# Kernel tuning notes

Measured on AMD Instinct MI355X. Metric: run time of the kernel, lower is better.

Reference implementation:

```python
import jax, jax.numpy as jnp
import numpy as np


def setup_inputs() -> dict:
    key = jax.random.key(0)
    B, T, N = 64, 256, 64
    inputs = jax.random.normal(key, (B, T, N), dtype=jnp.float32)
    return {"inputs": inputs}


def reference(inputs):
    # inputs: (B, T, N). Faithful to the TF layer: kendall_tau receives
    # x = inputs[:, :, i] of shape (B, T) and broadcasts over the BATCH axis,
    # so concordant = sum_{a,b,t} sign(x[a,t]-x[b,t]) * sign(y[a,t]-y[b,t])
    # and pairs = B*(B-1)//2. The scalar distance is written identically for
    # every batch entry at (i,j) and (j,i); the diagonal stays zero.
    B, T, N = inputs.shape
    # Sign of pairwise batch differences: (B, B, T, N)
    S = jnp.sign(inputs[None, :, :, :] - inputs[:, None, :, :])
    # Concordant counts for all asset pairs at once: Gram over (a, b, t)
    C = jnp.einsum('abti,abtj->ij', S, S)  # (N, N)
    pairs = jnp.asarray((B * (B - 1)) // 2, dtype=inputs.dtype)
    D = 1.0 - C / pairs
    # Diagonal entries are never written in the original loop (i < j) -> 0
    D = D * (1.0 - jnp.eye(N, dtype=inputs.dtype))
    # Same distance matrix tiled across the batch dimension
    return jnp.broadcast_to(D[None, :, :], (B, N, N))
```

## Files before the change

### kernel.cpp

```cpp
#include <hip/hip_runtime.h>
#include <stdint.h>

constexpr int B = 64, T = 256, N = 64;
constexpr int DW = 32;
constexpr int WPC = T * DW;
constexpr int SRC = 512;

__global__ __launch_bounds__(256) void kd_pack(const float* __restrict__ x,
                                               uint64_t* __restrict__ G) {
    __shared__ float V[64 * 65];
    int t  = blockIdx.x >> 2;
    int iq = blockIdx.x & 3;
    int tid = threadIdx.x;
    {
        int a = tid >> 2, seg = tid & 3;
        const float4* xg = (const float4*)x;
        size_t base = ((size_t)a * T + t) * (N / 4);
#pragma unroll
        for (int s = 0; s < 4; ++s) {
            float4 v4 = xg[base + seg * 4 + s];
            int off = a * 65 + seg * 16 + s * 4;
            V[off + 0] = v4.x; V[off + 1] = v4.y;
            V[off + 2] = v4.z; V[off + 3] = v4.w;
        }
    }
    __syncthreads();

    int w = tid >> 6, lane = tid & 63;
#pragma unroll
    for (int ii = 0; ii < 4; ++ii) {
        int i = iq * 16 + w * 4 + ii;
        float v = V[lane * 65 + i];
        uint64_t wv = 0;
#pragma unroll
        for (int d = 1; d <= 32; ++d) {
            float vr = __shfl(v, (lane + d) & 63, 64);
            uint64_t m = __ballot(vr > v);
            if (d == 32) m &= 0xffffffffull;
            if (lane == d - 1) wv = m;
        }
        if (lane < 32)
            G[(size_t)i * WPC + t * DW + lane] = wv;
    }
}

__global__ __launch_bounds__(256) void kd_gram(const uint64_t* __restrict__ G,
                                               int* __restrict__ part) {
    __shared__ uint64_t LG[16 * 66];
    int t = blockIdx.x >> 1, dh = blockIdx.x & 1;
    int tid = threadIdx.x;
    int base = t * DW + dh * 16;
    {
        int i = tid >> 2, k = tid & 3;
        const ulonglong2* gp = (const ulonglong2*)(G + (size_t)i * WPC + base);
        ulonglong2 v0 = gp[k * 2], v1 = gp[k * 2 + 1];
        LG[(4 * k + 0) * 66 + i] = v0.x;
        LG[(4 * k + 1) * 66 + i] = v0.y;
        LG[(4 * k + 2) * 66 + i] = v1.x;
        LG[(4 * k + 3) * 66 + i] = v1.y;
    }
    __syncthreads();

    const ulonglong2* LGv = (const ulonglong2*)LG;
    int i0 = (tid >> 4) * 4, j0 = (tid & 15) * 4;
    int acc[4][4] = {};
#pragma unroll
    for (int d = 0; d < 16; ++d) {
        ulonglong2 A0 = LGv[d * 33 + (i0 >> 1)];
        ulonglong2 A1 = LGv[d * 33 + (i0 >> 1) + 1];
        ulonglong2 B0 = LGv[d * 33 + (j0 >> 1)];
        ulonglong2 B1 = LGv[d * 33 + (j0 >> 1) + 1];
        uint64_t gi[4] = {A0.x, A0.y, A1.x, A1.y};
        uint64_t gj[4] = {B0.x, B0.y, B1.x, B1.y};
#pragma unroll
        for (int u = 0; u < 4; ++u)
#pragma unroll
            for (int v = 0; v < 4; ++v)
                acc[u][v] += (int)__popcll(gi[u] ^ gj[v]);
    }
    int* po = part + (size_t)blockIdx.x * (N * N);
#pragma unroll
    for (int u = 0; u < 4; ++u)
#pragma unroll
        for (int v = 0; v < 4; ++v)
            po[(i0 + u) * N + (j0 + v)] = acc[u][v];
}

__global__ __launch_bounds__(256) void kd_reduce(const int* __restrict__ part,
                                                 float* __restrict__ Dmat) {
    __shared__ int R[4][64];
    int b = blockIdx.x, tid = threadIdx.x;
    int c = b * 64 + (tid & 63);
    int sg = tid >> 6;
    int acc = 0;
    for (int s = sg; s < SRC; s += 4)
        acc += part[(size_t)s * (N * N) + c];
    R[sg][tid & 63] = acc;
    __syncthreads();
    if (tid < 64) {
        int X = R[0][tid] + R[1][tid] + R[2][tid] + R[3][tid];
        Dmat[b * 64 + tid] = (float)X * (1.0f / 504.0f) - 511.0f;
    }
}

__global__ __launch_bounds__(256) void kd_bcast(const float* __restrict__ Dmat,
                                                float* __restrict__ out) {
    int idx = blockIdx.x * 256 + threadIdx.x;
    int ij = idx & (N * N - 1);
    int i = ij >> 6, j = ij & 63;
    out[idx] = (i == j) ? 0.0f : Dmat[ij];
}

extern "C" void kernel_launch(void* const* d_in, const int* in_sizes, int n_in,
                              void* d_out, int out_size, void* d_ws, size_t ws_size,
                              hipStream_t stream) {
    const float* x = (const float*)d_in[0];
    float* out = (float*)d_out;

    uint64_t* G = (uint64_t*)d_ws;
    int* part = (int*)(G + (size_t)N * WPC);
    float* Dmat = (float*)(part + (size_t)SRC * (N * N));

    kd_pack<<<T * 4, 256, 0, stream>>>(x, G);
    kd_gram<<<SRC, 256, 0, stream>>>(G, part);
    kd_reduce<<<64, 256, 0, stream>>>(part, Dmat);
    kd_bcast<<<(B * N * N) / 256, 256, 0, stream>>>(Dmat, out);
}
```

Before: 93.18 us.

## Fuse sign-bit packing with popcount Gram and merge reduce with broadcast

Packs sign bits and runs the popcount Gram in a single kernel per time step, with 512 threads each handling one asset lane and four diagonal offsets, so the bit words never round-trip through a global buffer. Each thread builds its comparison masks in registers from 128 strided loads, replacing the shuffle/ballot scheme. The reduce and broadcast kernels are merged so the diagonal zeroing and the batch-wide writes happen straight from shared memory. This cuts two launches and the global G traffic, but the register arrays r/s[64] add heavy register pressure and the per-lane loads are strided by T*N.

```diff
diff --git a/kernel.cpp b/kernel.cpp
--- a/kernel.cpp
+++ b/kernel.cpp
@@ -2,70 +2,48 @@
 #include <stdint.h>
 
 constexpr int B = 64, T = 256, N = 64;
-constexpr int DW = 32;
-constexpr int WPC = T * DW;
-constexpr int SRC = 512;
+constexpr int NPART = T * 2;
 
-__global__ __launch_bounds__(256) void kd_pack(const float* __restrict__ x,
-                                               uint64_t* __restrict__ G) {
-    __shared__ float V[64 * 65];
-    int t  = blockIdx.x >> 2;
-    int iq = blockIdx.x & 3;
+__global__ __launch_bounds__(512) void kd_fused(const float* __restrict__ x,
+                                                int* __restrict__ part) {
+    __shared__ uint64_t LG[32 * 66];
+    int t = blockIdx.x;
     int tid = threadIdx.x;
+    int lane = tid & 63;
+    int w    = tid >> 6;
+    int rot  = w * 4;
+
     {
-        int a = tid >> 2, seg = tid & 3;
-        const float4* xg = (const float4*)x;
-        size_t base = ((size_t)a * T + t) * (N / 4);
+        const float* xb = x + (size_t)t * N + lane;
+        float r[64], s[64];
 #pragma unroll
-        for (int s = 0; s < 4; ++s) {
-            float4 v4 = xg[base + seg * 4 + s];
-            int off = a * 65 + seg * 16 + s * 4;
-            V[off + 0] = v4.x; V[off + 1] = v4.y;
-            V[off + 2] = v4.z; V[off + 3] = v4.w;
+        for (int a = 0; a < 64; ++a)
+            r[a] = xb[(size_t)a * (T * N)];
+#pragma unroll
+        for (int a = 0; a < 64; ++a)
+            s[a] = xb[(size_t)((a + rot) & 63) * (T * N)];
+
+#pragma unroll
+        for (int k = 0; k < 4; ++k) {
+            uint64_t gw = 0;
+#pragma unroll
+            for (int a = 0; a < 64; ++a)
+                gw |= (uint64_t)(s[(a + k + 1) & 63] > r[a]) << a;
+            int dslot = rot + k;
+            if (dslot == 31) gw &= 0xffffffffull;
+            LG[dslot * 66 + lane] = gw;
         }
     }
     __syncthreads();
 
-    int w = tid >> 6, lane = tid & 63;
-#pragma unroll
-    for (int ii = 0; ii < 4; ++ii) {
-        int i = iq * 16 + w * 4 + ii;
-        float v = V[lane * 65 + i];
-        uint64_t wv = 0;
-#pragma unroll
-        for (int d = 1; d <= 32; ++d) {
-            float vr = __shfl(v, (lane + d) & 63, 64);
-            uint64_t m = __ballot(vr > v);
-            if (d == 32) m &= 0xffffffffull;
-            if (lane == d - 1) wv = m;
-        }
-        if (lane < 32)
-            G[(size_t)i * WPC + t * DW + lane] = wv;
-    }
-}
-
-__global__ __launch_bounds__(256) void kd_gram(const uint64_t* __restrict__ G,
-                                               int* __restrict__ part) {
-    __shared__ uint64_t LG[16 * 66];
-    int t = blockIdx.x >> 1, dh = blockIdx.x & 1;
-    int tid = threadIdx.x;
-    int base = t * DW + dh * 16;
-    {
-        int i = tid >> 2, k = tid & 3;
-        const ulonglong2* gp = (const ulonglong2*)(G + (size_t)i * WPC + base);
-        ulonglong2 v0 = gp[k * 2], v1 = gp[k * 2 + 1];
-        LG[(4 * k + 0) * 66 + i] = v0.x;
-        LG[(4 * k + 1) * 66 + i] = v0.y;
-        LG[(4 * k + 2) * 66 + i] = v1.x;
-        LG[(4 * k + 3) * 66 + i] = v1.y;
-    }
-    __syncthreads();
-
+    int half = tid >> 8;
+    int t2 = tid & 255;
+    int i0 = (t2 >> 4) * 4, j0 = (t2 & 15) * 4;
     const ulonglong2* LGv = (const ulonglong2*)LG;
-    int i0 = (tid >> 4) * 4, j0 = (tid & 15) * 4;
     int acc[4][4] = {};
 #pragma unroll
-    for (int d = 0; d < 16; ++d) {
+    for (int dd = 0; dd < 16; ++dd) {
+        int d = half * 16 + dd;
         ulonglong2 A0 = LGv[d * 33 + (i0 >> 1)];
         ulonglong2 A1 = LGv[d * 33 + (i0 >> 1) + 1];
         ulonglong2 B0 = LGv[d * 33 + (j0 >> 1)];
@@ -78,7 +56,7 @@
             for (int v = 0; v < 4; ++v)
                 acc[u][v] += (int)__popcll(gi[u] ^ gj[v]);
     }
-    int* po = part + (size_t)blockIdx.x * (N * N);
+    int* po = part + ((size_t)t * 2 + half) * (N * N);
 #pragma unroll
     for (int u = 0; u < 4; ++u)
 #pragma unroll
@@ -86,29 +64,27 @@
             po[(i0 + u) * N + (j0 + v)] = acc[u][v];
 }
 
-__global__ __launch_bounds__(256) void kd_reduce(const int* __restrict__ part,
-                                                 float* __restrict__ Dmat) {
+__global__ __launch_bounds__(256) void kd_out(const int* __restrict__ part,
+                                              float* __restrict__ out) {
     __shared__ int R[4][64];
+    __shared__ float Dv[64];
     int b = blockIdx.x, tid = threadIdx.x;
-    int c = b * 64 + (tid & 63);
-    int sg = tid >> 6;
+    int l = tid & 63, sg = tid >> 6;
     int acc = 0;
-    for (int s = sg; s < SRC; s += 4)
-        acc += part[(size_t)s * (N * N) + c];
-    R[sg][tid & 63] = acc;
+    for (int s = sg; s < NPART; s += 4)
+        acc += part[(size_t)s * (N * N) + b * 64 + l];
+    R[sg][l] = acc;
     __syncthreads();
     if (tid < 64) {
         int X = R[0][tid] + R[1][tid] + R[2][tid] + R[3][tid];
-        Dmat[b * 64 + tid] = (float)X * (1.0f / 504.0f) - 511.0f;
+        Dv[tid] = (tid == b) ? 0.0f : ((float)X * (1.0f / 504.0f) - 511.0f);
     }
-}
-
-__global__ __launch_bounds__(256) void kd_bcast(const float* __restrict__ Dmat,
-                                                float* __restrict__ out) {
-    int idx = blockIdx.x * 256 + threadIdx.x;
-    int ij = idx & (N * N - 1);
-    int i = ij >> 6, j = ij & 63;
-    out[idx] = (i == j) ? 0.0f : Dmat[ij];
+    __syncthreads();
+#pragma unroll
+    for (int it = 0; it < 16; ++it) {
+        int batch = it * 4 + sg;
+        out[(size_t)batch * (N * N) + b * 64 + l] = Dv[l];
+    }
 }
 
 extern "C" void kernel_launch(void* const* d_in, const int* in_sizes, int n_in,
@@ -117,12 +93,8 @@
     const float* x = (const float*)d_in[0];
     float* out = (float*)d_out;
 
-    uint64_t* G = (uint64_t*)d_ws;
-    int* part = (int*)(G + (size_t)N * WPC);
-    float* Dmat = (float*)(part + (size_t)SRC * (N * N));
+    int* part = (int*)d_ws;
 
-    kd_pack<<<T * 4, 256, 0, stream>>>(x, G);
-    kd_gram<<<SRC, 256, 0, stream>>>(G, part);
-    kd_reduce<<<64, 256, 0, stream>>>(part, Dmat);
-    kd_bcast<<<(B * N * N) / 256, 256, 0, stream>>>(Dmat, out);
+    kd_fused<<<T, 512, 0, stream>>>(x, part);
+    kd_out<<<N, 256, 0, stream>>>(part, out);
 }
```

New measurement: 82.54 us. -11.4%, faster.
